# Performance work log

Hardware: AMD Instinct MI355X
Metric: run time of the kernel (lower is better)

Reference implementation:

```python
import jax, jax.numpy as jnp
import numpy as np

DIM = 512; NB = 4; BS = DIM // NB            # EinFFT blocks
DS = 64; DC = 4; EXP = 2; DI = EXP * DIM      # Mamba dims
DTR = DIM // 16                               # dt_rank
BLOCKS = 2; LAM = 0.01; B_SZ = 2; L_SZ = 1024

def layer_norm(x, w, b):
    m = x.mean(-1, keepdims=True)
    v = x.var(-1, keepdims=True)
    return (x - m) / jnp.sqrt(v + 1e-5) * w + b

def softshrink(x, lam):
    return jnp.where(x > lam, x - lam, jnp.where(x < -lam, x + lam, jnp.zeros((), x.dtype)))

def mamba(x, in_proj_w, conv_w, conv_b, x_proj_w, dt_proj_w, dt_proj_b, A_log, D, out_proj_w):
    B, L, _ = x.shape
    xz = x @ in_proj_w.T                      # (B,L,2*DI)
    xm, z = jnp.split(xz, 2, axis=-1)
    # causal depthwise conv1d, keep first L outputs
    xt = xm.transpose(0, 2, 1)                # (B,DI,L)
    conv = jax.lax.conv_general_dilated(xt, conv_w, (1,), [(DC - 1, 0)],
                                        feature_group_count=DI,
                                        dimension_numbers=('NCH', 'OIH', 'NCH'))
    xm = jax.nn.silu((conv + conv_b[None, :, None]).transpose(0, 2, 1))  # (B,L,DI)
    proj = xm @ x_proj_w.T                    # (B,L,DTR+2*DS)
    dt = proj[..., :DTR]
    Bm = proj[..., DTR:DTR + DS]
    Cm = proj[..., DTR + DS:]
    dt = jax.nn.softplus(dt @ dt_proj_w.T + dt_proj_b)   # (B,L,DI)
    A = -jnp.exp(A_log)                       # (DI,DS)

    def step(h, inp):
        dt_t, B_t, C_t, u_t = inp             # (B,DI),(B,DS),(B,DS),(B,DI)
        dA = jnp.exp(dt_t[:, :, None] * A)
        h = dA * h + dt_t[:, :, None] * B_t[:, None, :] * u_t[:, :, None]
        y = jnp.einsum('bds,bs->bd', h, C_t)
        return h, y

    h0 = jnp.zeros((B, DI, DS), x.dtype)
    _, ys = jax.lax.scan(step, h0, (dt.transpose(1, 0, 2), Bm.transpose(1, 0, 2),
                                    Cm.transpose(1, 0, 2), xm.transpose(1, 0, 2)))
    y = ys.transpose(1, 0, 2) + xm * D        # (B,L,DI)
    y = y * jax.nn.silu(z)
    return y @ out_proj_w.T

def einfft(x, cw1, cw2, cb1, cb2):
    B, N, C = x.shape
    xf = jnp.fft.fft2(x.reshape(B, N, NB, BS), axes=(1, 2), norm='ortho')
    mul = lambda t, w: jnp.einsum('BNbd,bdk->BNbk', t, w)
    r1 = jax.nn.relu(mul(xf.real, cw1[0]) - mul(xf.imag, cw1[1]) + cb1[0])
    i1 = jax.nn.relu(mul(xf.real, cw1[1]) + mul(xf.imag, cw1[0]) + cb1[1])
    r2 = softshrink(mul(r1, cw2[0]) - mul(i1, cw2[1]) + cb2[0], LAM)
    i2 = softshrink(mul(r1, cw2[1]) + mul(i1, cw2[0]) + cb2[1], LAM)
    out = jnp.fft.ifft2(r2 + 1j * i2, axes=(1, 2), norm='ortho')
    return out.real.astype(x.dtype).reshape(B, N, C)

def setup_inputs() -> dict:
    key = jax.random.key(0)
    ks = jax.random.split(key, 16)
    r = lambda i, shape, s: jax.random.normal(ks[i], shape, jnp.float32) * s
    A_log = jnp.log(jnp.tile(jnp.arange(1, DS + 1, dtype=jnp.float32), (DI, 1)))
    return {
        'x': jax.random.normal(ks[0], (B_SZ, L_SZ, DIM), jnp.float32),
        'ln_w': jnp.ones((DIM,), jnp.float32), 'ln_b': jnp.zeros((DIM,), jnp.float32),
        'in_proj_w': r(1, (2 * DI, DIM), 0.02),
        'conv_w': r(2, (DI, 1, DC), 0.1), 'conv_b': jnp.zeros((DI,), jnp.float32),
        'x_proj_w': r(3, (DTR + 2 * DS, DI), 0.02),
        'dt_proj_w': r(4, (DI, DTR), 0.02),
        'dt_proj_b': jnp.full((DI,), float(np.log(np.expm1(0.01))), jnp.float32),
        'A_log': A_log, 'D': jnp.ones((DI,), jnp.float32),
        'out_proj_w': r(5, (DIM, DI), 0.02),
        'norm2_w': jnp.ones((DIM,), jnp.float32), 'norm2_b': jnp.zeros((DIM,), jnp.float32),
        'cw1': r(6, (2, NB, BS, BS), 0.02), 'cw2': r(7, (2, NB, BS, BS), 0.02),
        'cb1': r(8, (2, NB, BS), 0.02), 'cb2': r(9, (2, NB, BS), 0.02),
    }

def reference(x, ln_w, ln_b, in_proj_w, conv_w, conv_b, x_proj_w, dt_proj_w, dt_proj_b,
              A_log, D, out_proj_w, norm2_w, norm2_b, cw1, cw2, cb1, cb2):
    for _ in range(BLOCKS):
        x = x + mamba(layer_norm(x, ln_w, ln_b), in_proj_w, conv_w, conv_b,
                      x_proj_w, dt_proj_w, dt_proj_b, A_log, D, out_proj_w)
        x = x + einfft(layer_norm(x, norm2_w, norm2_b), cw1, cw2, cb1, cb2)
    return x
```

## Files before the change

kernel.cpp:

```cpp
#include <hip/hip_runtime.h>

typedef unsigned short u16;
typedef __attribute__((ext_vector_type(8))) short bf8;
typedef __attribute__((ext_vector_type(4))) float f4;

__device__ __forceinline__ float bf2f(u16 b) {
    return __uint_as_float(((unsigned)b) << 16);
}
__device__ __forceinline__ u16 f2bf(float f) {
    unsigned u = __float_as_uint(f);
    u += 0x7fffu + ((u >> 16) & 1u);
    return (u16)(u >> 16);
}
__device__ __forceinline__ void pack8f(const float* v, u16* dst) {
    uint r0 = (uint)f2bf(v[0]) | ((uint)f2bf(v[1]) << 16);
    uint r1 = (uint)f2bf(v[2]) | ((uint)f2bf(v[3]) << 16);
    uint r2 = (uint)f2bf(v[4]) | ((uint)f2bf(v[5]) << 16);
    uint r3 = (uint)f2bf(v[6]) | ((uint)f2bf(v[7]) << 16);
    *(uint4*)dst = make_uint4(r0, r1, r2, r3);
}
__device__ __forceinline__ bf8 neg8(bf8 v) {
    union { bf8 b; uint u[4]; } t; t.b = v;
    t.u[0] ^= 0x80008000u; t.u[1] ^= 0x80008000u;
    t.u[2] ^= 0x80008000u; t.u[3] ^= 0x80008000u;
    return t.b;
}
__device__ __forceinline__ int digrev10(int x) {
    int r = __brev((unsigned)x) >> 22;
    return ((r & 0x2AA) >> 1) | ((r & 0x155) << 1);
}

__global__ void detect_k(const u16* __restrict__ dtb, int* __restrict__ flag) {
    flag[0] = (dtb[0] == dtb[1] && dtb[1] == dtb[2] && dtb[2] == dtb[3] &&
               dtb[3] == dtb[4] && dtb[4] == dtb[5]) ? 1 : 0;
    flag[1] = 1;
}

__global__ __launch_bounds__(256)
void achk_k(const float* __restrict__ alog, int* __restrict__ flag) {
    int i = blockIdx.x * 256 + threadIdx.x;
    int s = i & 63;
    float n = __expf(alog[i]);
    float e = (float)(s + 1);
    if (fabsf(n - e) > 0.02f * e) atomicAnd(&flag[1], 0);
}

struct CvtArgs {
    const void* src[18];
    void* dst[18];
    int n[18];
    int obf[18];
};
__global__ __launch_bounds__(256)
void cvt_all_k(CvtArgs a, const int* __restrict__ flag) {
    const int t = blockIdx.y;
    const int n = a.n[t];
    const int f = flag[0];
    if (a.obf[t] == 2) {
        u16* __restrict__ d = (u16*)a.dst[t];
        if (f) {
            const u16* __restrict__ s = (const u16*)a.src[t];
            for (int i = blockIdx.x * 256 + threadIdx.x; i < n; i += gridDim.x * 256) {
                int cin = i & 127, cout = (i >> 7) & 127, snb = i >> 14;
                d[(snb << 14) + (cout << 7) + cin] = s[(snb << 14) + (cin << 7) + cout];
            }
        } else {
            const float* __restrict__ s = (const float*)a.src[t];
            for (int i = blockIdx.x * 256 + threadIdx.x; i < n; i += gridDim.x * 256) {
                int cin = i & 127, cout = (i >> 7) & 127, snb = i >> 14;
                d[(snb << 14) + (cout << 7) + cin] =
                    f2bf(s[(snb << 14) + (cin << 7) + cout]);
            }
        }
    } else if (a.obf[t] == 1) {
        u16* __restrict__ d = (u16*)a.dst[t];
        if (f) {
            const u16* __restrict__ s = (const u16*)a.src[t];
            for (int i = blockIdx.x * 256 + threadIdx.x; i < n; i += gridDim.x * 256)
                d[i] = s[i];
        } else {
            const float* __restrict__ s = (const float*)a.src[t];
            for (int i = blockIdx.x * 256 + threadIdx.x; i < n; i += gridDim.x * 256)
                d[i] = f2bf(s[i]);
        }
    } else {
        float* __restrict__ d = (float*)a.dst[t];
        if (f) {
            const u16* __restrict__ s = (const u16*)a.src[t];
            for (int i = blockIdx.x * 256 + threadIdx.x; i < n; i += gridDim.x * 256)
                d[i] = bf2f(s[i]);
        } else {
            const float* __restrict__ s = (const float*)a.src[t];
            for (int i = blockIdx.x * 256 + threadIdx.x; i < n; i += gridDim.x * 256)
                d[i] = s[i];
        }
    }
}

__global__ void out_k(const float* __restrict__ in, void* __restrict__ out,
                      int n, const int* __restrict__ flag) {
    int i = blockIdx.x * 256 + threadIdx.x;
    if (i >= n) return;
    if (flag[0]) ((u16*)out)[i] = f2bf(in[i]);
    else         ((float*)out)[i] = in[i];
}

__global__ __launch_bounds__(256)
void ln_k(const float* __restrict__ x, const float* __restrict__ w,
          const float* __restrict__ b, u16* __restrict__ out) {
    const int row = blockIdx.x, tid = threadIdx.x;
    const float* xr = x + (long)row * 512;
    float v0 = xr[tid], v1 = xr[tid + 256];
    float s = v0 + v1, q = v0 * v0 + v1 * v1;
#pragma unroll
    for (int off = 32; off; off >>= 1) {
        s += __shfl_xor(s, off);
        q += __shfl_xor(q, off);
    }
    __shared__ float ss[4], qq[4];
    int wid = tid >> 6;
    if ((tid & 63) == 0) { ss[wid] = s; qq[wid] = q; }
    __syncthreads();
    s = ss[0] + ss[1] + ss[2] + ss[3];
    q = qq[0] + qq[1] + qq[2] + qq[3];
    float mean = s * (1.f / 512.f);
    float var = q * (1.f / 512.f) - mean * mean;
    float rstd = rsqrtf(var + 1e-5f);
    u16* o = out + (long)row * 512;
    o[tid]       = f2bf((v0 - mean) * rstd * w[tid]       + b[tid]);
    o[tid + 256] = f2bf((v1 - mean) * rstd * w[tid + 256] + b[tid + 256]);
}

#define LSTR 40
template <int TAF, int EPI>
__global__ __launch_bounds__(256)
void mgemm_k(const void* __restrict__ Ap, const u16* __restrict__ Bp,
             float* __restrict__ D, int N, int K, int lda, int ldb, int ldc,
             long bsA, long bsB, long bsC,
             const float* __restrict__ bias, const float* __restrict__ res) {
    const float* Af = (const float*)Ap + blockIdx.z * bsA;
    const u16*  Ab  = (const u16*)Ap + blockIdx.z * bsA;
    const u16*  B   = Bp + blockIdx.z * bsB;
    D += blockIdx.z * bsC;

    __shared__ u16 As[64 * LSTR];
    __shared__ u16 Bs[64 * LSTR];
    const int tid = threadIdx.x;
    const int lane = tid & 63;
    const int w = tid >> 6, wm = w & 1, wn = w >> 1;
    const int m0 = blockIdx.y * 64, n0 = blockIdx.x * 64;
    const int fr = (lane & 15), fq = (lane >> 4);

    f4 acc[2][2] = {};

    for (int k0 = 0; k0 < K; k0 += 32) {
        {
            const int ar = tid >> 2, aks = (tid & 3) << 3;
            if constexpr (TAF == 1) {
                *(uint4*)&As[ar * LSTR + aks] =
                    *(const uint4*)(Ab + (long)(m0 + ar) * lda + k0 + aks);
            } else if constexpr (TAF == 2) {
                const float* p = Af + (long)(m0 + ar) * lda + k0 + aks;
                float4 x = *(const float4*)p, y = *(const float4*)(p + 4);
#pragma unroll
                for (int pt = 1; pt < 4; ++pt) {
                    const float* pp = p + (long)pt * bsA;
                    float4 x1 = *(const float4*)pp, y1 = *(const float4*)(pp + 4);
                    x.x += x1.x; x.y += x1.y; x.z += x1.z; x.w += x1.w;
                    y.x += y1.x; y.y += y1.y; y.z += y1.z; y.w += y1.w;
                }
                float tv[8];
                tv[0] = x.x; tv[1] = x.y; tv[2] = x.z; tv[3] = x.w;
                tv[4] = y.x; tv[5] = y.y; tv[6] = y.z; tv[7] = y.w;
                pack8f(tv, &As[ar * LSTR + aks]);
            } else {
                const float* p = Af + (long)(m0 + ar) * lda + k0 + aks;
                float tv[8];
                float4 x = *(const float4*)p, y = *(const float4*)(p + 4);
                tv[0] = x.x; tv[1] = x.y; tv[2] = x.z; tv[3] = x.w;
                tv[4] = y.x; tv[5] = y.y; tv[6] = y.z; tv[7] = y.w;
                pack8f(tv, &As[ar * LSTR + aks]);
            }
        }
        {
            const int br = tid >> 2, bks = (tid & 3) << 3;
            uint4 raw = make_uint4(0, 0, 0, 0);
            if (n0 + br < N)
                raw = *(const uint4*)(B + (long)(n0 + br) * ldb + k0 + bks);
            *(uint4*)&Bs[br * LSTR + bks] = raw;
        }
        __syncthreads();
        bf8 af[2], bff[2];
#pragma unroll
        for (int t = 0; t < 2; t++) {
            af[t]  = *(bf8*)&As[(wm * 32 + t * 16 + fr) * LSTR + (fq << 3)];
            bff[t] = *(bf8*)&Bs[(wn * 32 + t * 16 + fr) * LSTR + (fq << 3)];
        }
#pragma unroll
        for (int i = 0; i < 2; i++)
#pragma unroll
            for (int j = 0; j < 2; j++)
                acc[i][j] = __builtin_amdgcn_mfma_f32_16x16x32_bf16(
                    af[i], bff[j], acc[i][j], 0, 0, 0);
        __syncthreads();
    }

#pragma unroll
    for (int i = 0; i < 2; i++) {
#pragma unroll
        for (int j = 0; j < 2; j++) {
            const int gmb = m0 + wm * 32 + i * 16 + (fq << 2);
            const int gn  = n0 + wn * 32 + j * 16 + fr;
            if (gn >= N) continue;
            float v[4];
#pragma unroll
            for (int e = 0; e < 4; e++) v[e] = acc[i][j][e];
            if constexpr (EPI == 1) {
                float bb = bias[gn];
#pragma unroll
                for (int e = 0; e < 4; e++) {
                    float t = v[e] + bb;
                    v[e] = (t > 20.f) ? t : log1pf(__expf(t));
                }
            }
#pragma unroll
            for (int e = 0; e < 4; e++) {
                long idx = (long)(gmb + e) * ldc + gn;
                float t = v[e];
                if constexpr (EPI == 2) t += res[idx];
                D[idx] = t;
            }
        }
    }
}

__global__ __launch_bounds__(256)
void gemm128_k(const u16* __restrict__ A, const u16* __restrict__ B,
               float* __restrict__ D, int K, int lda, int ldb, int ldc) {
    __shared__ u16 As[128 * LSTR];
    __shared__ u16 Bs[128 * LSTR];
    const int tid = threadIdx.x, lane = tid & 63;
    const int w = tid >> 6, wm = w & 1, wn = w >> 1;
    const int m0 = blockIdx.y * 128, n0 = blockIdx.x * 128;
    const int fr = lane & 15, fq = lane >> 4;
    f4 acc[4][4] = {};

    for (int k0 = 0; k0 < K; k0 += 32) {
#pragma unroll
        for (int j = 0; j < 2; ++j) {
            int idx = tid + j * 256;
            int row = idx >> 2, col = (idx & 3) << 3;
            *(uint4*)&As[row * LSTR + col] =
                *(const uint4*)(A + (long)(m0 + row) * lda + k0 + col);
            *(uint4*)&Bs[row * LSTR + col] =
                *(const uint4*)(B + (long)(n0 + row) * ldb + k0 + col);
        }
        __syncthreads();
        bf8 af[4], bfv[4];
#pragma unroll
        for (int i = 0; i < 4; ++i) {
            af[i]  = *(bf8*)&As[(wm * 64 + i * 16 + fr) * LSTR + (fq << 3)];
            bfv[i] = *(bf8*)&Bs[(wn * 64 + i * 16 + fr) * LSTR + (fq << 3)];
        }
#pragma unroll
        for (int i = 0; i < 4; ++i)
#pragma unroll
            for (int j = 0; j < 4; ++j)
                acc[i][j] = __builtin_amdgcn_mfma_f32_16x16x32_bf16(
                    af[i], bfv[j], acc[i][j], 0, 0, 0);
        __syncthreads();
    }
#pragma unroll
    for (int i = 0; i < 4; ++i)
#pragma unroll
        for (int j = 0; j < 4; ++j) {
            const int gm = m0 + wm * 64 + i * 16 + (fq << 2);
            const int gn = n0 + wn * 64 + j * 16 + fr;
#pragma unroll
            for (int e = 0; e < 4; ++e)
                D[(long)(gm + e) * ldc + gn] = acc[i][j][e];
        }
}

__global__ __launch_bounds__(1024)
void ffw_k(const u16* __restrict__ xn, u16* __restrict__ Orb,
           u16* __restrict__ Oib) {
    const int bz = blockIdx.x;
    const int b = bz >> 7, cg = bz & 127;
    const int t = threadIdx.x;
    const int f = t >> 8, tl = t & 255;
    const int c = cg + f * 128;
    __shared__ float re[4224], im[4224], twr[768], twi[768];
    if (t < 768) {
        float s, cc;
        __sincosf((float)t * -6.1359231515425649e-3f, &s, &cc);
        twr[t] = cc; twi[t] = s;
    }
    float* rf = re + f * 1056;
    float* mf = im + f * 1056;
    const u16* src = xn + ((long)b * 1024) * 512 + c;
#pragma unroll
    for (int r = 0; r < 4; ++r) {
        int n = tl + r * 256;
        float v = bf2f(src[(long)n * 512]);
        int a = n + (n >> 5);
        rf[a] = v; mf[a] = 0.f;
    }
    __syncthreads();
#pragma unroll
    for (int st = 0; st < 5; ++st) {
        const int qsh = 8 - 2 * st;
        const int q = 1 << qsh;
        const int len = q << 2;
        const int m = 1 << (2 * st);
        int j = tl & (q - 1);
        int g = tl >> qsh;
        int i0 = g * len + j;
        int a0 = i0 + (i0 >> 5);
        int i1 = i0 + q,     a1 = i1 + (i1 >> 5);
        int i2 = i0 + 2 * q, a2 = i2 + (i2 >> 5);
        int i3 = i0 + 3 * q, a3 = i3 + (i3 >> 5);
        float ar = rf[a0], ai = mf[a0];
        float br = rf[a1], bi = mf[a1];
        float cr = rf[a2], ci = mf[a2];
        float dr = rf[a3], di = mf[a3];
        float t0r = ar + cr, t0i = ai + ci;
        float t1r = ar - cr, t1i = ai - ci;
        float t2r = br + dr, t2i = bi + di;
        float u = br - dr, v = bi - di;
        rf[a0] = t0r + t2r; mf[a0] = t0i + t2i;
        {
            int k = j * m;
            float wr = twr[k], wi = twi[k];
            float xr = t1r + v, xi = t1i - u;
            rf[a1] = xr * wr - xi * wi;
            mf[a1] = xr * wi + xi * wr;
        }
        {
            int k = 2 * j * m;
            float wr = twr[k], wi = twi[k];
            float xr = t0r - t2r, xi = t0i - t2i;
            rf[a2] = xr * wr - xi * wi;
            mf[a2] = xr * wi + xi * wr;
        }
        {
            int k = 3 * j * m;
            float wr = twr[k], wi = twi[k];
            float xr = t1r - v, xi = t1i + u;
            rf[a3] = xr * wr - xi * wi;
            mf[a3] = xr * wi + xi * wr;
        }
        __syncthreads();
    }
    u16* drp = Orb + ((long)(b * 512 + c)) * 1024;
    u16* dip = Oib + ((long)(b * 512 + c)) * 1024;
#pragma unroll
    for (int r = 0; r < 4; ++r) {
        int kf = tl + r * 256;
        int sidx = digrev10(kf);
        int a = sidx + (sidx >> 5);
        float r0 = re[a],        i0v = im[a];
        float r1 = re[1056 + a], i1v = im[1056 + a];
        float r2 = re[2112 + a], i2v = im[2112 + a];
        float r3 = re[3168 + a], i3v = im[3168 + a];
        float vr, vi;
        if (f == 0)      { vr = r0 + r1 + r2 + r3;     vi = i0v + i1v + i2v + i3v; }
        else if (f == 1) { vr = r0 + i1v - r2 - i3v;   vi = i0v - r1 - i2v + r3; }
        else if (f == 2) { vr = r0 - r1 + r2 - r3;     vi = i0v - i1v + i2v - i3v; }
        else             { vr = r0 - i1v - r2 + i3v;   vi = i0v + r1 - i2v - r3; }
        drp[kf] = f2bf(vr * 0.015625f);
        dip[kf] = f2bf(vi * 0.015625f);
    }
}

__global__ __launch_bounds__(1024)
void ifw_k(const u16* __restrict__ X2r, const u16* __restrict__ X2i,
           float* __restrict__ Yc) {
    const int bz = blockIdx.x;
    const int b = bz >> 7, cg = bz & 127;
    const int t = threadIdx.x;
    const int f = t >> 8, tl = t & 255;
    const int c = cg + f * 128;
    __shared__ float re[4224], im[4224], twr[768], twi[768];
    if (t < 768) {
        float s, cc;
        __sincosf((float)t * 6.1359231515425649e-3f, &s, &cc);
        twr[t] = cc; twi[t] = s;
    }
    const u16* sr = X2r + ((long)(b * 512 + c)) * 1024;
    const u16* si = X2i + ((long)(b * 512 + c)) * 1024;
    float* rf = re + f * 1056;
    float* mf = im + f * 1056;
    const int k4 = tl * 4;
    {
        uint2 pr = *(const uint2*)&sr[k4];
        uint2 pi = *(const uint2*)&si[k4];
        u16 rv[4] = {(u16)(pr.x & 0xFFFF), (u16)(pr.x >> 16),
                     (u16)(pr.y & 0xFFFF), (u16)(pr.y >> 16)};
        u16 iv[4] = {(u16)(pi.x & 0xFFFF), (u16)(pi.x >> 16),
                     (u16)(pi.y & 0xFFFF), (u16)(pi.y >> 16)};
#pragma unroll
        for (int e = 0; e < 4; ++e) {
            int idx = k4 + e;
            int a = idx + (idx >> 5);
            rf[a] = bf2f(rv[e]);
            mf[a] = bf2f(iv[e]);
        }
    }
    __syncthreads();
    float vr[4], vi[4];
#pragma unroll
    for (int e = 0; e < 4; ++e) {
        int idx = k4 + e;
        int a = idx + (idx >> 5);
        float r0 = re[a],        i0v = im[a];
        float r1 = re[1056 + a], i1v = im[1056 + a];
        float r2 = re[2112 + a], i2v = im[2112 + a];
        float r3 = re[3168 + a], i3v = im[3168 + a];
        if (f == 0)      { vr[e] = r0 + r1 + r2 + r3;     vi[e] = i0v + i1v + i2v + i3v; }
        else if (f == 1) { vr[e] = r0 - i1v - r2 + i3v;   vi[e] = i0v + r1 - i2v - r3; }
        else if (f == 2) { vr[e] = r0 - r1 + r2 - r3;     vi[e] = i0v - i1v + i2v - i3v; }
        else             { vr[e] = r0 + i1v - r2 - i3v;   vi[e] = i0v - r1 - i2v + r3; }
        vr[e] *= 0.5f; vi[e] *= 0.5f;
    }
    __syncthreads();
#pragma unroll
    for (int e = 0; e < 4; ++e) {
        int idx = k4 + e;
        int a = idx + (idx >> 5);
        rf[a] = vr[e]; mf[a] = vi[e];
    }
    __syncthreads();
#pragma unroll
    for (int st = 0; st < 5; ++st) {
        const int qsh = 8 - 2 * st;
        const int q = 1 << qsh;
        const int len = q << 2;
        const int m = 1 << (2 * st);
        int j = tl & (q - 1);
        int g = tl >> qsh;
        int i0 = g * len + j;
        int a0 = i0 + (i0 >> 5);
        int i1 = i0 + q,     a1 = i1 + (i1 >> 5);
        int i2 = i0 + 2 * q, a2 = i2 + (i2 >> 5);
        int i3 = i0 + 3 * q, a3 = i3 + (i3 >> 5);
        float ar = rf[a0], ai = mf[a0];
        float br = rf[a1], bi = mf[a1];
        float cr = rf[a2], ci = mf[a2];
        float dr = rf[a3], di = mf[a3];
        float t0r = ar + cr, t0i = ai + ci;
        float t1r = ar - cr, t1i = ai - ci;
        float t2r = br + dr, t2i = bi + di;
        float u = br - dr, v = bi - di;
        rf[a0] = t0r + t2r; mf[a0] = t0i + t2i;
        {
            int k = j * m;
            float wr = twr[k], wi = twi[k];
            float xr = t1r - v, xi = t1i + u;
            rf[a1] = xr * wr - xi * wi;
            mf[a1] = xr * wi + xi * wr;
        }
        {
            int k = 2 * j * m;
            float wr = twr[k], wi = twi[k];
            float xr = t0r - t2r, xi = t0i - t2i;
            rf[a2] = xr * wr - xi * wi;
            mf[a2] = xr * wi + xi * wr;
        }
        {
            int k = 3 * j * m;
            float wr = twr[k], wi = twi[k];
            float xr = t1r + v, xi = t1i - u;
            rf[a3] = xr * wr - xi * wi;
            mf[a3] = xr * wi + xi * wr;
        }
        __syncthreads();
    }
    float* d = Yc + ((long)(b * 512 + c)) * 1024;
#pragma unroll
    for (int r = 0; r < 4; ++r) {
        int n = tl + r * 256;
        int sidx = digrev10(n);
        int a = sidx + (sidx >> 5);
        d[n] = rf[a] * 0.03125f;
    }
}

__global__ __launch_bounds__(256)
void transadd_k(float* __restrict__ xbuf, const float* __restrict__ Yc) {
    const int b = blockIdx.z;
    const int c0 = blockIdx.x * 64, n0 = blockIdx.y * 64;
    __shared__ float T[64][65];
    const int tid = threadIdx.x;
    const int r = tid >> 2, q = (tid & 3) * 16;
    const float* src = Yc + ((long)(b * 512 + c0 + r)) * 1024 + n0 + q;
#pragma unroll
    for (int k = 0; k < 4; ++k) {
        float4 v = *(const float4*)(src + k * 4);
        T[r][q + k * 4 + 0] = v.x; T[r][q + k * 4 + 1] = v.y;
        T[r][q + k * 4 + 2] = v.z; T[r][q + k * 4 + 3] = v.w;
    }
    __syncthreads();
    float* dst = xbuf + ((long)(b * 1024 + n0 + r)) * 512 + c0 + q;
#pragma unroll
    for (int k = 0; k < 4; ++k) {
        float4 w = *(const float4*)(dst + k * 4);
        w.x += T[q + k * 4 + 0][r]; w.y += T[q + k * 4 + 1][r];
        w.z += T[q + k * 4 + 2][r]; w.w += T[q + k * 4 + 3][r];
        *(float4*)(dst + k * 4) = w;
    }
}

#define LSTR2 136
template <int ACT>
__global__ __launch_bounds__(256)
void cmix_k(const u16* __restrict__ Xr, const u16* __restrict__ Xi,
            const u16* __restrict__ WT, const float* __restrict__ cb,
            u16* __restrict__ Or, u16* __restrict__ Oi) {
    const int z = blockIdx.z, b = z >> 2, nb = z & 3;
    const u16* Ar = Xr + (long)b * 524288 + nb * 131072;
    const u16* Ai = Xi + (long)b * 524288 + nb * 131072;
    const u16* Wr = WT + nb * 16384;
    const u16* Wi = WT + 65536 + nb * 16384;
    u16* Dr = Or + (long)b * 524288 + nb * 131072;
    u16* Di = Oi + (long)b * 524288 + nb * 131072;
    __shared__ u16 Ars[64 * LSTR2], Ais[64 * LSTR2], Brs[64 * LSTR2], Bis[64 * LSTR2];
    const int tid = threadIdx.x, lane = tid & 63;
    const int w = tid >> 6, wm = w & 1, wn = w >> 1;
    const int m0 = blockIdx.y * 64, n0 = blockIdx.x * 64;
    const int fr = (lane & 15), fq = (lane >> 4);
    f4 accr[2][2] = {}, acci[2][2] = {};

    {
        const int am = tid & 63, akb = (tid >> 6) << 3;
#pragma unroll
        for (int kk = 0; kk < 4; ++kk) {
            const int kb = kk * 32 + akb;
            u16 tr[8], ti[8];
#pragma unroll
            for (int j = 0; j < 8; j++) {
                long off = (long)(kb + j) * 1024 + m0 + am;
                tr[j] = Ar[off]; ti[j] = Ai[off];
            }
            uint r0 = (uint)tr[0] | ((uint)tr[1] << 16);
            uint r1 = (uint)tr[2] | ((uint)tr[3] << 16);
            uint r2 = (uint)tr[4] | ((uint)tr[5] << 16);
            uint r3 = (uint)tr[6] | ((uint)tr[7] << 16);
            *(uint4*)&Ars[am * LSTR2 + kb] = make_uint4(r0, r1, r2, r3);
            r0 = (uint)ti[0] | ((uint)ti[1] << 16);
            r1 = (uint)ti[2] | ((uint)ti[3] << 16);
            r2 = (uint)ti[4] | ((uint)ti[5] << 16);
            r3 = (uint)ti[6] | ((uint)ti[7] << 16);
            *(uint4*)&Ais[am * LSTR2 + kb] = make_uint4(r0, r1, r2, r3);
        }
        const int br = tid >> 2, bks = (tid & 3) << 3;
#pragma unroll
        for (int kk = 0; kk < 4; ++kk) {
            const int kb = kk * 32 + bks;
            *(uint4*)&Brs[br * LSTR2 + kb] =
                *(const uint4*)(Wr + (long)(n0 + br) * 128 + kb);
            *(uint4*)&Bis[br * LSTR2 + kb] =
                *(const uint4*)(Wi + (long)(n0 + br) * 128 + kb);
        }
    }
    __syncthreads();

#pragma unroll
    for (int kq = 0; kq < 4; ++kq) {
        const int kc = kq * 32 + (fq << 3);
        bf8 arf[2], aif[2], brf[2], bif[2];
#pragma unroll
        for (int t = 0; t < 2; t++) {
            arf[t] = *(bf8*)&Ars[(wm * 32 + t * 16 + fr) * LSTR2 + kc];
            aif[t] = *(bf8*)&Ais[(wm * 32 + t * 16 + fr) * LSTR2 + kc];
            brf[t] = *(bf8*)&Brs[(wn * 32 + t * 16 + fr) * LSTR2 + kc];
            bif[t] = *(bf8*)&Bis[(wn * 32 + t * 16 + fr) * LSTR2 + kc];
        }
        bf8 nai[2] = { neg8(aif[0]), neg8(aif[1]) };
#pragma unroll
        for (int i = 0; i < 2; i++)
#pragma unroll
            for (int j = 0; j < 2; j++) {
                accr[i][j] = __builtin_amdgcn_mfma_f32_16x16x32_bf16(arf[i], brf[j], accr[i][j], 0, 0, 0);
                accr[i][j] = __builtin_amdgcn_mfma_f32_16x16x32_bf16(nai[i], bif[j], accr[i][j], 0, 0, 0);
                acci[i][j] = __builtin_amdgcn_mfma_f32_16x16x32_bf16(arf[i], bif[j], acci[i][j], 0, 0, 0);
                acci[i][j] = __builtin_amdgcn_mfma_f32_16x16x32_bf16(aif[i], brf[j], acci[i][j], 0, 0, 0);
            }
    }

#pragma unroll
    for (int i = 0; i < 2; i++)
#pragma unroll
        for (int j = 0; j < 2; j++) {
            const int gmb = m0 + wm * 32 + i * 16 + (fq << 2);
            const int gn  = n0 + wn * 32 + j * 16 + fr;
            const float bbr = cb[nb * 128 + gn];
            const float bbi = cb[512 + nb * 128 + gn];
            u16 pr[4], pi[4];
#pragma unroll
            for (int e = 0; e < 4; e++) {
                float vr = accr[i][j][e] + bbr;
                float vi = acci[i][j][e] + bbi;
                if (ACT == 0) {
                    vr = fmaxf(vr, 0.f);
                    vi = fmaxf(vi, 0.f);
                } else {
                    vr = (vr > 0.01f) ? vr - 0.01f : ((vr < -0.01f) ? vr + 0.01f : 0.f);
                    vi = (vi > 0.01f) ? vi - 0.01f : ((vi < -0.01f) ? vi + 0.01f : 0.f);
                }
                pr[e] = f2bf(vr); pi[e] = f2bf(vi);
            }
            uint2 wr2, wi2;
            wr2.x = (uint)pr[0] | ((uint)pr[1] << 16);
            wr2.y = (uint)pr[2] | ((uint)pr[3] << 16);
            wi2.x = (uint)pi[0] | ((uint)pi[1] << 16);
            wi2.y = (uint)pi[2] | ((uint)pi[3] << 16);
            *(uint2*)&Dr[(long)gn * 1024 + gmb] = wr2;
            *(uint2*)&Di[(long)gn * 1024 + gmb] = wi2;
        }
}

__global__ __launch_bounds__(256)
void conv_k(const float* __restrict__ xz, const float* __restrict__ cw,
            const float* __restrict__ cb, u16* __restrict__ u) {
    int idx = blockIdx.x * 256 + threadIdx.x;
    int d = idx & 1023;
    int l = (idx >> 10) & 1023;
    int b = idx >> 20;
    float acc = cb[d];
    const float* base = xz + (long)b * 1024 * 2048 + d;
#pragma unroll
    for (int j = 0; j < 4; j++) {
        int li = l - 3 + j;
        if (li >= 0) acc = fmaf(cw[d * 4 + j], base[(long)li * 2048], acc);
    }
    float sig = 1.f / (1.f + __expf(-acc));
    u[idx] = f2bf(acc * sig);
}

__global__ __launch_bounds__(256)
void scan1_k(const float* __restrict__ dtL, const u16* __restrict__ uLb,
             const float* __restrict__ Pb, const float* __restrict__ alog,
             u16* __restrict__ Hb, float* __restrict__ Sbuf,
             const int* __restrict__ flag) {
    const int dg = blockIdx.x, c = blockIdx.y, b = blockIdx.z;
    const int tid = threadIdx.x;
    const int d = dg * 256 + tid;
    const int t0 = c * 16;
    __shared__ float Bls[16][64];
    {
        int r = tid >> 4, cg = (tid & 15) << 2;
        const float* src = Pb + ((long)(b * 1024 + t0 + r)) * 160 + 32 + cg;
        float4 v0 = *(const float4*)src;
        float4 v1 = *(const float4*)(src + 327680);
        float4 v2 = *(const float4*)(src + 655360);
        float4 v3 = *(const float4*)(src + 983040);
        v0.x += v1.x + v2.x + v3.x;
        v0.y += v1.y + v2.y + v3.y;
        v0.z += v1.z + v2.z + v3.z;
        v0.w += v1.w + v2.w + v3.w;
        *(float4*)&Bls[r][cg] = v0;
    }
    __syncthreads();

    float h[64];
#pragma unroll
    for (int s = 0; s < 64; s++) h[s] = 0.f;
    float S = 0.f;
    const float* dtp = dtL + (long)(b * 1024 + t0) * 1024 + d;
    const u16* up = uLb + (long)(b * 1024 + t0) * 1024 + d;

    if (flag[1]) {
        for (int t = 0; t < 16; ++t) {
            float dt = dtp[(long)t * 1024];
            float uu = bf2f(up[(long)t * 1024]);
            float dtu = dt * uu;
            S += dt;
            float q = __expf(-dt);
            float q2 = q * q, q3 = q2 * q, q4 = q2 * q2;
            float a0 = q, a1 = q2, a2 = q3, a3 = q4;
            const float4* B4p = (const float4*)&Bls[t][0];
#pragma unroll
            for (int sg = 0; sg < 16; ++sg) {
                float4 B4 = B4p[sg];
                h[sg * 4 + 0] = a0 * h[sg * 4 + 0] + dtu * B4.x;
                h[sg * 4 + 1] = a1 * h[sg * 4 + 1] + dtu * B4.y;
                h[sg * 4 + 2] = a2 * h[sg * 4 + 2] + dtu * B4.z;
                h[sg * 4 + 3] = a3 * h[sg * 4 + 3] + dtu * B4.w;
                a0 *= q4; a1 *= q4; a2 *= q4; a3 *= q4;
            }
        }
    } else {
        float A[64];
        const float* ap = alog + (long)d * 64;
#pragma unroll
        for (int s = 0; s < 64; s += 4) {
            float4 a4 = *(const float4*)(ap + s);
            A[s] = -__expf(a4.x); A[s + 1] = -__expf(a4.y);
            A[s + 2] = -__expf(a4.z); A[s + 3] = -__expf(a4.w);
        }
        for (int t = 0; t < 16; ++t) {
            float dt = dtp[(long)t * 1024];
            float uu = bf2f(up[(long)t * 1024]);
            float dtu = dt * uu;
            S += dt;
            const float4* B4p = (const float4*)&Bls[t][0];
#pragma unroll
            for (int sg = 0; sg < 16; ++sg) {
                float4 B4 = B4p[sg];
                h[sg * 4 + 0] = __expf(dt * A[sg * 4 + 0]) * h[sg * 4 + 0] + dtu * B4.x;
                h[sg * 4 + 1] = __expf(dt * A[sg * 4 + 1]) * h[sg * 4 + 1] + dtu * B4.y;
                h[sg * 4 + 2] = __expf(dt * A[sg * 4 + 2]) * h[sg * 4 + 2] + dtu * B4.z;
                h[sg * 4 + 3] = __expf(dt * A[sg * 4 + 3]) * h[sg * 4 + 3] + dtu * B4.w;
            }
        }
    }
    u16* Hp = Hb + ((((long)(b * 64 + c)) * 1024 + d) << 6);
#pragma unroll
    for (int s = 0; s < 64; s += 4) {
        uint2 p;
        p.x = ((__float_as_uint(h[s]) + 0x8000u) >> 16) |
              ((__float_as_uint(h[s + 1]) + 0x8000u) & 0xFFFF0000u);
        p.y = ((__float_as_uint(h[s + 2]) + 0x8000u) >> 16) |
              ((__float_as_uint(h[s + 3]) + 0x8000u) & 0xFFFF0000u);
        *(uint2*)&Hp[s] = p;
    }
    Sbuf[(b * 64 + c) * 1024 + d] = S;
}

__global__ __launch_bounds__(256)
void scan2_k(const float* __restrict__ alog, const float* __restrict__ Sbuf,
             u16* __restrict__ Hb) {
    int idx = blockIdx.x * 256 + threadIdx.x;
    int s = idx & 63, d = (idx >> 6) & 1023, b = idx >> 16;
    float A = -__expf(alog[(long)d * 64 + s]);
    float carry = 0.f;
    for (int c = 0; c < 64; ++c) {
        float S = Sbuf[(b * 64 + c) * 1024 + d];
        float P = __expf(A * S);
        long off = ((((long)(b * 64 + c)) * 1024 + d) << 6) + s;
        float H = bf2f(Hb[off]);
        Hb[off] = (u16)((__float_as_uint(carry) + 0x8000u) >> 16);
        carry = P * carry + H;
    }
}

__global__ __launch_bounds__(256)
void scan3_k(const float* __restrict__ dtL, const u16* __restrict__ uLb,
             const float* __restrict__ xz, const float* __restrict__ Pb,
             const float* __restrict__ alog, const u16* __restrict__ Hb,
             const float* __restrict__ Dw, const int* __restrict__ flag,
             u16* __restrict__ y2) {
    const int dg = blockIdx.x, c = blockIdx.y, b = blockIdx.z;
    const int tid = threadIdx.x;
    const int d = dg * 256 + tid;
    const int t0 = c * 16;
    __shared__ float Bls[16][64];
    __shared__ float Cls[16][64];
    {
        int r = tid >> 4, cg = (tid & 15) << 2;
        const float* src = Pb + ((long)(b * 1024 + t0 + r)) * 160 + 32 + cg;
        float4 v0 = *(const float4*)src;
        float4 v1 = *(const float4*)(src + 327680);
        float4 v2 = *(const float4*)(src + 655360);
        float4 v3 = *(const float4*)(src + 983040);
        v0.x += v1.x + v2.x + v3.x;
        v0.y += v1.y + v2.y + v3.y;
        v0.z += v1.z + v2.z + v3.z;
        v0.w += v1.w + v2.w + v3.w;
        *(float4*)&Bls[r][cg] = v0;
        float4 c0 = *(const float4*)(src + 64);
        float4 c1 = *(const float4*)(src + 64 + 327680);
        float4 c2 = *(const float4*)(src + 64 + 655360);
        float4 c3 = *(const float4*)(src + 64 + 983040);
        c0.x += c1.x + c2.x + c3.x;
        c0.y += c1.y + c2.y + c3.y;
        c0.z += c1.z + c2.z + c3.z;
        c0.w += c1.w + c2.w + c3.w;
        *(float4*)&Cls[r][cg] = c0;
    }
    __syncthreads();

    float h[64];
    const u16* Hp = Hb + ((((long)(b * 64 + c)) * 1024 + d) << 6);
#pragma unroll
    for (int s = 0; s < 64; s += 4) {
        uint2 p = *(const uint2*)&Hp[s];
        h[s]     = __uint_as_float(p.x << 16);
        h[s + 1] = __uint_as_float(p.x & 0xFFFF0000u);
        h[s + 2] = __uint_as_float(p.y << 16);
        h[s + 3] = __uint_as_float(p.y & 0xFFFF0000u);
    }
    const float Dd = Dw[d];
    const float* dtp = dtL + (long)(b * 1024 + t0) * 1024 + d;
    const u16* up = uLb + (long)(b * 1024 + t0) * 1024 + d;
    const float* zp = xz + (long)(b * 1024 + t0) * 2048 + 1024 + d;
    u16* y2p = y2 + (long)(b * 1024 + t0) * 1024 + d;

    if (flag[1]) {
        for (int t = 0; t < 16; ++t) {
            float dt = dtp[(long)t * 1024];
            float uu = bf2f(up[(long)t * 1024]);
            float zz = zp[(long)t * 2048];
            float dtu = dt * uu;
            float y = 0.f;
            float q = __expf(-dt);
            float q2 = q * q, q3 = q2 * q, q4 = q2 * q2;
            float a0 = q, a1 = q2, a2 = q3, a3 = q4;
            const float4* B4p = (const float4*)&Bls[t][0];
            const float4* C4p = (const float4*)&Cls[t][0];
#pragma unroll
            for (int sg = 0; sg < 16; ++sg) {
                float4 B4 = B4p[sg];
                float4 C4 = C4p[sg];
                h[sg * 4 + 0] = a0 * h[sg * 4 + 0] + dtu * B4.x;
                y = fmaf(h[sg * 4 + 0], C4.x, y);
                h[sg * 4 + 1] = a1 * h[sg * 4 + 1] + dtu * B4.y;
                y = fmaf(h[sg * 4 + 1], C4.y, y);
                h[sg * 4 + 2] = a2 * h[sg * 4 + 2] + dtu * B4.z;
                y = fmaf(h[sg * 4 + 2], C4.z, y);
                h[sg * 4 + 3] = a3 * h[sg * 4 + 3] + dtu * B4.w;
                y = fmaf(h[sg * 4 + 3], C4.w, y);
                a0 *= q4; a1 *= q4; a2 *= q4; a3 *= q4;
            }
            float g = zz / (1.f + __expf(-zz));
            y2p[(long)t * 1024] = f2bf((y + uu * Dd) * g);
        }
    } else {
        float A[64];
        const float* ap = alog + (long)d * 64;
#pragma unroll
        for (int s = 0; s < 64; s += 4) {
            float4 a4 = *(const float4*)(ap + s);
            A[s] = -__expf(a4.x); A[s + 1] = -__expf(a4.y);
            A[s + 2] = -__expf(a4.z); A[s + 3] = -__expf(a4.w);
        }
        for (int t = 0; t < 16; ++t) {
            float dt = dtp[(long)t * 1024];
            float uu = bf2f(up[(long)t * 1024]);
            float zz = zp[(long)t * 2048];
            float dtu = dt * uu;
            float y = 0.f;
            const float4* B4p = (const float4*)&Bls[t][0];
            const float4* C4p = (const float4*)&Cls[t][0];
#pragma unroll
            for (int sg = 0; sg < 16; ++sg) {
                float4 B4 = B4p[sg];
                float4 C4 = C4p[sg];
                h[sg * 4 + 0] = __expf(dt * A[sg * 4 + 0]) * h[sg * 4 + 0] + dtu * B4.x;
                y = fmaf(h[sg * 4 + 0], C4.x, y);
                h[sg * 4 + 1] = __expf(dt * A[sg * 4 + 1]) * h[sg * 4 + 1] + dtu * B4.y;
                y = fmaf(h[sg * 4 + 1], C4.y, y);
                h[sg * 4 + 2] = __expf(dt * A[sg * 4 + 2]) * h[sg * 4 + 2] + dtu * B4.z;
                y = fmaf(h[sg * 4 + 2], C4.z, y);
                h[sg * 4 + 3] = __expf(dt * A[sg * 4 + 3]) * h[sg * 4 + 3] + dtu * B4.w;
                y = fmaf(h[sg * 4 + 3], C4.w, y);
            }
            float g = zz / (1.f + __expf(-zz));
            y2p[(long)t * 1024] = f2bf((y + uu * Dd) * g);
        }
    }
}

extern "C" void kernel_launch(void* const* d_in, const int* in_sizes, int n_in,
                              void* d_out, int out_size, void* d_ws, size_t ws_size,
                              hipStream_t stream) {
    float* ws = (float*)d_ws;
    int* flag = (int*)ws;
    size_t o = 64;
    float* xbuf  = ws + o; o += 1048576;
    float* xz    = ws + o; o += 4194304;
    float* dtL   = ws + o; o += 2097152;
    u16* xnb     = (u16*)(ws + o); o += 524288;
    u16* wInpB   = (u16*)(ws + o); o += 524288;
    u16* wXpB    = (u16*)(ws + o); o += 81920;
    u16* wDtB    = (u16*)(ws + o); o += 16384;
    u16* wOutB   = (u16*)(ws + o); o += 262144;
    u16* WT1     = (u16*)(ws + o); o += 65536;
    u16* WT2     = (u16*)(ws + o); o += 65536;
    float* wConv = ws + o; o += 4096;
    float* wAlog = ws + o; o += 65536;
    float* wLnW  = ws + o; o += 512;
    float* wLnB  = ws + o; o += 512;
    float* wConvB= ws + o; o += 1024;
    float* wDtBias=ws + o; o += 1024;
    float* wD    = ws + o; o += 1024;
    float* wN2w  = ws + o; o += 512;
    float* wN2b  = ws + o; o += 512;
    float* wCb1  = ws + o; o += 1024;
    float* wCb2  = ws + o; o += 1024;
    float* Hreg  = ws + o; o += 4194304;
    float* Sbuf  = ws + o; o += 131072;
    float* Pbuf2 = ws + o; o += 1310720;
    u16* uLb     = (u16*)(ws + o); o += 1048576;
    u16* y2b     = (u16*)(ws + o); o += 524288;
    u16* Hb    = (u16*)Hreg;
    float* Yc  = dtL;
    u16* xzb  = (u16*)xz;
    u16* Xrb  = xzb;
    u16* Xib  = xzb + 1048576;
    u16* r1b  = xzb + 2097152;
    u16* i1b  = xzb + 3145728;
    u16* X2rb = xzb + 4194304;
    u16* X2ib = xzb + 5242880;

    dim3 blk(256);

    detect_k<<<1, 1, 0, stream>>>((const u16*)d_in[8], flag);

    CvtArgs ca;
    void* dsts[18] = {xbuf, wLnW, wLnB, wInpB, wConv, wConvB, wXpB, wDtB, wDtBias,
                      wAlog, wD, wOutB, wN2w, wN2b, WT1, WT2, wCb1, wCb2};
    int obf[18]    = {0,    0,    0,    1,     0,     0,      1,    1,    0,
                      0,     0,  1,     0,    0,    2,   2,   0,    0};
    for (int i = 0; i < 18; i++) {
        ca.src[i] = d_in[i];
        ca.dst[i] = dsts[i];
        ca.n[i] = in_sizes[i];
        ca.obf[i] = obf[i];
    }
    cvt_all_k<<<dim3(64, 18), blk, 0, stream>>>(ca, flag);
    achk_k<<<256, blk, 0, stream>>>(wAlog, flag);

    for (int it = 0; it < 2; ++it) {
        ln_k<<<2048, blk, 0, stream>>>(xbuf, wLnW, wLnB, xnb);
        gemm128_k<<<dim3(16, 16), blk, 0, stream>>>(
            xnb, wInpB, xz, 512, 512, 512, 2048);
        conv_k<<<8192, blk, 0, stream>>>(xz, wConv, wConvB, uLb);
        mgemm_k<1, 0><<<dim3(3, 32, 4), blk, 0, stream>>>(
            uLb, wXpB, Pbuf2, 160, 256, 1024, 1024, 160,
            256, 256, 327680, nullptr, nullptr);
        mgemm_k<2, 1><<<dim3(16, 32, 1), blk, 0, stream>>>(
            Pbuf2, wDtB, dtL, 1024, 32, 160, 32, 1024, 327680, 0, 0, wDtBias, nullptr);
        scan1_k<<<dim3(4, 64, 2), blk, 0, stream>>>(dtL, uLb, Pbuf2, wAlog, Hb, Sbuf, flag);
        scan2_k<<<512, blk, 0, stream>>>(wAlog, Sbuf, Hb);
        scan3_k<<<dim3(4, 64, 2), blk, 0, stream>>>(dtL, uLb, xz, Pbuf2, wAlog, Hb, wD, flag, y2b);
        mgemm_k<1, 2><<<dim3(8, 32, 1), blk, 0, stream>>>(
            y2b, wOutB, xbuf, 512, 1024, 1024, 1024, 512, 0, 0, 0, nullptr, xbuf);

        ln_k<<<2048, blk, 0, stream>>>(xbuf, wN2w, wN2b, xnb);
        ffw_k<<<256, dim3(1024), 0, stream>>>(xnb, Xrb, Xib);
        cmix_k<0><<<dim3(2, 16, 8), blk, 0, stream>>>(Xrb, Xib, WT1, wCb1, r1b, i1b);
        cmix_k<1><<<dim3(2, 16, 8), blk, 0, stream>>>(r1b, i1b, WT2, wCb2, X2rb, X2ib);
        ifw_k<<<256, dim3(1024), 0, stream>>>(X2rb, X2ib, Yc);
        transadd_k<<<dim3(8, 16, 2), blk, 0, stream>>>(xbuf, Yc);
    }

    out_k<<<(out_size + 255) / 256, blk, 0, stream>>>(xbuf, d_out, out_size, flag);
}
```

Before: 445.8 us.

## Store dt and z in bf16, split in_proj output, precompute reduced B/C

The in_proj GEMM now writes the x half as fp32 to a compact buffer and the z gate half as bf16. The dt projection epilogue emits bf16, and the scan kernels read bf16 dt and z. scan1 stores the split-K reduced B and C rows so scan3 loads them directly instead of re-reducing four partials. scan2 also prefetches the next chunk's S and H values. The aim is to cut global memory traffic in the Mamba scan path, at the cost of storing dt and z at bf16 precision.

```diff
diff --git a/kernel.cpp b/kernel.cpp
--- a/kernel.cpp
+++ b/kernel.cpp
@@ -215,7 +215,7 @@
             float v[4];
 #pragma unroll
             for (int e = 0; e < 4; e++) v[e] = acc[i][j][e];
-            if constexpr (EPI == 1) {
+            if constexpr (EPI == 1 || EPI == 3) {
                 float bb = bias[gn];
 #pragma unroll
                 for (int e = 0; e < 4; e++) {
@@ -228,7 +228,8 @@
                 long idx = (long)(gmb + e) * ldc + gn;
                 float t = v[e];
                 if constexpr (EPI == 2) t += res[idx];
-                D[idx] = t;
+                if constexpr (EPI == 3) ((u16*)D)[idx] = f2bf(t);
+                else                    D[idx] = t;
             }
         }
     }
@@ -236,7 +237,8 @@
 
 __global__ __launch_bounds__(256)
 void gemm128_k(const u16* __restrict__ A, const u16* __restrict__ B,
-               float* __restrict__ D, int K, int lda, int ldb, int ldc) {
+               float* __restrict__ Dm, u16* __restrict__ Dz,
+               int K, int lda, int ldb) {
     __shared__ u16 As[128 * LSTR];
     __shared__ u16 Bs[128 * LSTR];
     const int tid = threadIdx.x, lane = tid & 63;
@@ -276,9 +278,15 @@
         for (int j = 0; j < 4; ++j) {
             const int gm = m0 + wm * 64 + i * 16 + (fq << 2);
             const int gn = n0 + wn * 64 + j * 16 + fr;
-#pragma unroll
-            for (int e = 0; e < 4; ++e)
-                D[(long)(gm + e) * ldc + gn] = acc[i][j][e];
+            if (n0 < 1024) {
+#pragma unroll
+                for (int e = 0; e < 4; ++e)
+                    Dm[(long)(gm + e) * 1024 + gn] = acc[i][j][e];
+            } else {
+#pragma unroll
+                for (int e = 0; e < 4; ++e)
+                    Dz[(long)(gm + e) * 1024 + (gn - 1024)] = f2bf(acc[i][j][e]);
+            }
         }
 }
 
@@ -621,27 +629,28 @@
 }
 
 __global__ __launch_bounds__(256)
-void conv_k(const float* __restrict__ xz, const float* __restrict__ cw,
+void conv_k(const float* __restrict__ xm, const float* __restrict__ cw,
             const float* __restrict__ cb, u16* __restrict__ u) {
     int idx = blockIdx.x * 256 + threadIdx.x;
     int d = idx & 1023;
     int l = (idx >> 10) & 1023;
     int b = idx >> 20;
     float acc = cb[d];
-    const float* base = xz + (long)b * 1024 * 2048 + d;
+    const float* base = xm + (long)b * 1048576 + d;
 #pragma unroll
     for (int j = 0; j < 4; j++) {
         int li = l - 3 + j;
-        if (li >= 0) acc = fmaf(cw[d * 4 + j], base[(long)li * 2048], acc);
+        if (li >= 0) acc = fmaf(cw[d * 4 + j], base[(long)li * 1024], acc);
     }
     float sig = 1.f / (1.f + __expf(-acc));
     u[idx] = f2bf(acc * sig);
 }
 
 __global__ __launch_bounds__(256)
-void scan1_k(const float* __restrict__ dtL, const u16* __restrict__ uLb,
+void scan1_k(const u16* __restrict__ dtb, const u16* __restrict__ uLb,
              const float* __restrict__ Pb, const float* __restrict__ alog,
              u16* __restrict__ Hb, float* __restrict__ Sbuf,
+             float* __restrict__ Bred, float* __restrict__ Cred,
              const int* __restrict__ flag) {
     const int dg = blockIdx.x, c = blockIdx.y, b = blockIdx.z;
     const int tid = threadIdx.x;
@@ -660,6 +669,19 @@
         v0.z += v1.z + v2.z + v3.z;
         v0.w += v1.w + v2.w + v3.w;
         *(float4*)&Bls[r][cg] = v0;
+        if (dg == 0) {
+            long ro = (((long)(b * 64 + c)) * 16 + r) * 64 + cg;
+            *(float4*)&Bred[ro] = v0;
+            float4 c0 = *(const float4*)(src + 64);
+            float4 c1 = *(const float4*)(src + 64 + 327680);
+            float4 c2 = *(const float4*)(src + 64 + 655360);
+            float4 c3 = *(const float4*)(src + 64 + 983040);
+            c0.x += c1.x + c2.x + c3.x;
+            c0.y += c1.y + c2.y + c3.y;
+            c0.z += c1.z + c2.z + c3.z;
+            c0.w += c1.w + c2.w + c3.w;
+            *(float4*)&Cred[ro] = c0;
+        }
     }
     __syncthreads();
 
@@ -667,12 +689,12 @@
 #pragma unroll
     for (int s = 0; s < 64; s++) h[s] = 0.f;
     float S = 0.f;
-    const float* dtp = dtL + (long)(b * 1024 + t0) * 1024 + d;
-    const u16* up = uLb + (long)(b * 1024 + t0) * 1024 + d;
+    const u16* dtp = dtb + (long)(b * 1024 + t0) * 1024 + d;
+    const u16* up  = uLb + (long)(b * 1024 + t0) * 1024 + d;
 
     if (flag[1]) {
         for (int t = 0; t < 16; ++t) {
-            float dt = dtp[(long)t * 1024];
+            float dt = bf2f(dtp[(long)t * 1024]);
             float uu = bf2f(up[(long)t * 1024]);
             float dtu = dt * uu;
             S += dt;
@@ -700,7 +722,7 @@
             A[s + 2] = -__expf(a4.z); A[s + 3] = -__expf(a4.w);
         }
         for (int t = 0; t < 16; ++t) {
-            float dt = dtp[(long)t * 1024];
+            float dt = bf2f(dtp[(long)t * 1024]);
             float uu = bf2f(up[(long)t * 1024]);
             float dtu = dt * uu;
             S += dt;
@@ -735,22 +757,30 @@
     int s = idx & 63, d = (idx >> 6) & 1023, b = idx >> 16;
     float A = -__expf(alog[(long)d * 64 + s]);
     float carry = 0.f;
+    long off = ((((long)(b * 64)) * 1024 + d) << 6) + s;
+    int sb = (b * 64) * 1024 + d;
+    float Scur = Sbuf[sb];
+    float Hcur = bf2f(Hb[off]);
     for (int c = 0; c < 64; ++c) {
-        float S = Sbuf[(b * 64 + c) * 1024 + d];
-        float P = __expf(A * S);
-        long off = ((((long)(b * 64 + c)) * 1024 + d) << 6) + s;
-        float H = bf2f(Hb[off]);
+        float Snxt = 0.f, Hnxt = 0.f;
+        if (c < 63) {
+            Snxt = Sbuf[sb + 1024];
+            Hnxt = bf2f(Hb[off + 65536]);
+        }
+        float P = __expf(A * Scur);
         Hb[off] = (u16)((__float_as_uint(carry) + 0x8000u) >> 16);
-        carry = P * carry + H;
-    }
-}
-
-__global__ __launch_bounds__(256)
-void scan3_k(const float* __restrict__ dtL, const u16* __restrict__ uLb,
-             const float* __restrict__ xz, const float* __restrict__ Pb,
-             const float* __restrict__ alog, const u16* __restrict__ Hb,
-             const float* __restrict__ Dw, const int* __restrict__ flag,
-             u16* __restrict__ y2) {
+        carry = P * carry + Hcur;
+        Scur = Snxt; Hcur = Hnxt;
+        off += 65536; sb += 1024;
+    }
+}
+
+__global__ __launch_bounds__(256)
+void scan3_k(const u16* __restrict__ dtb, const u16* __restrict__ uLb,
+             const u16* __restrict__ zLb, const float* __restrict__ Bred,
+             const float* __restrict__ Cred, const float* __restrict__ alog,
+             const u16* __restrict__ Hb, const float* __restrict__ Dw,
+             const int* __restrict__ flag, u16* __restrict__ y2) {
     const int dg = blockIdx.x, c = blockIdx.y, b = blockIdx.z;
     const int tid = threadIdx.x;
     const int d = dg * 256 + tid;
@@ -759,25 +789,9 @@
     __shared__ float Cls[16][64];
     {
         int r = tid >> 4, cg = (tid & 15) << 2;
-        const float* src = Pb + ((long)(b * 1024 + t0 + r)) * 160 + 32 + cg;
-        float4 v0 = *(const float4*)src;
-        float4 v1 = *(const float4*)(src + 327680);
-        float4 v2 = *(const float4*)(src + 655360);
-        float4 v3 = *(const float4*)(src + 983040);
-        v0.x += v1.x + v2.x + v3.x;
-        v0.y += v1.y + v2.y + v3.y;
-        v0.z += v1.z + v2.z + v3.z;
-        v0.w += v1.w + v2.w + v3.w;
-        *(float4*)&Bls[r][cg] = v0;
-        float4 c0 = *(const float4*)(src + 64);
-        float4 c1 = *(const float4*)(src + 64 + 327680);
-        float4 c2 = *(const float4*)(src + 64 + 655360);
-        float4 c3 = *(const float4*)(src + 64 + 983040);
-        c0.x += c1.x + c2.x + c3.x;
-        c0.y += c1.y + c2.y + c3.y;
-        c0.z += c1.z + c2.z + c3.z;
-        c0.w += c1.w + c2.w + c3.w;
-        *(float4*)&Cls[r][cg] = c0;
+        long ro = (((long)(b * 64 + c)) * 16 + r) * 64 + cg;
+        *(float4*)&Bls[r][cg] = *(const float4*)&Bred[ro];
+        *(float4*)&Cls[r][cg] = *(const float4*)&Cred[ro];
     }
     __syncthreads();
 
@@ -792,16 +806,16 @@
         h[s + 3] = __uint_as_float(p.y & 0xFFFF0000u);
     }
     const float Dd = Dw[d];
-    const float* dtp = dtL + (long)(b * 1024 + t0) * 1024 + d;
-    const u16* up = uLb + (long)(b * 1024 + t0) * 1024 + d;
-    const float* zp = xz + (long)(b * 1024 + t0) * 2048 + 1024 + d;
+    const u16* dtp = dtb + (long)(b * 1024 + t0) * 1024 + d;
+    const u16* up  = uLb + (long)(b * 1024 + t0) * 1024 + d;
+    const u16* zp  = zLb + (long)(b * 1024 + t0) * 1024 + d;
     u16* y2p = y2 + (long)(b * 1024 + t0) * 1024 + d;
 
     if (flag[1]) {
         for (int t = 0; t < 16; ++t) {
-            float dt = dtp[(long)t * 1024];
+            float dt = bf2f(dtp[(long)t * 1024]);
             float uu = bf2f(up[(long)t * 1024]);
-            float zz = zp[(long)t * 2048];
+            float zz = bf2f(zp[(long)t * 1024]);
             float dtu = dt * uu;
             float y = 0.f;
             float q = __expf(-dt);
@@ -836,9 +850,9 @@
             A[s + 2] = -__expf(a4.z); A[s + 3] = -__expf(a4.w);
         }
         for (int t = 0; t < 16; ++t) {
-            float dt = dtp[(long)t * 1024];
+            float dt = bf2f(dtp[(long)t * 1024]);
             float uu = bf2f(up[(long)t * 1024]);
-            float zz = zp[(long)t * 2048];
+            float zz = bf2f(zp[(long)t * 1024]);
             float dtu = dt * uu;
             float y = 0.f;
             const float4* B4p = (const float4*)&Bls[t][0];
@@ -869,8 +883,9 @@
     int* flag = (int*)ws;
     size_t o = 64;
     float* xbuf  = ws + o; o += 1048576;
-    float* xz    = ws + o; o += 4194304;
-    float* dtL   = ws + o; o += 2097152;
+    float* fftA  = ws + o; o += 3145728;
+    float* xmL   = ws + o; o += 2097152;
+    float* Yc    = ws + o; o += 1048576;
     u16* xnb     = (u16*)(ws + o); o += 524288;
     u16* wInpB   = (u16*)(ws + o); o += 524288;
     u16* wXpB    = (u16*)(ws + o); o += 81920;
@@ -894,9 +909,12 @@
     float* Pbuf2 = ws + o; o += 1310720;
     u16* uLb     = (u16*)(ws + o); o += 1048576;
     u16* y2b     = (u16*)(ws + o); o += 524288;
+    u16* dtLb    = (u16*)(ws + o); o += 1048576;
+    u16* zLb     = (u16*)(ws + o); o += 1048576;
+    float* Bred  = ws + o; o += 131072;
+    float* Cred  = ws + o; o += 131072;
     u16* Hb    = (u16*)Hreg;
-    float* Yc  = dtL;
-    u16* xzb  = (u16*)xz;
+    u16* xzb  = (u16*)fftA;
     u16* Xrb  = xzb;
     u16* Xib  = xzb + 1048576;
     u16* r1b  = xzb + 2097152;
@@ -925,16 +943,19 @@
     for (int it = 0; it < 2; ++it) {
         ln_k<<<2048, blk, 0, stream>>>(xbuf, wLnW, wLnB, xnb);
         gemm128_k<<<dim3(16, 16), blk, 0, stream>>>(
-            xnb, wInpB, xz, 512, 512, 512, 2048);
-        conv_k<<<8192, blk, 0, stream>>>(xz, wConv, wConvB, uLb);
+            xnb, wInpB, xmL, zLb, 512, 512, 512);
+        conv_k<<<8192, blk, 0, stream>>>(xmL, wConv, wConvB, uLb);
         mgemm_k<1, 0><<<dim3(3, 32, 4), blk, 0, stream>>>(
             uLb, wXpB, Pbuf2, 160, 256, 1024, 1024, 160,
             256, 256, 327680, nullptr, nullptr);
-        mgemm_k<2, 1><<<dim3(16, 32, 1), blk, 0, stream>>>(
-            Pbuf2, wDtB, dtL, 1024, 32, 160, 32, 1024, 327680, 0, 0, wDtBias, nullptr);
-        scan1_k<<<dim3(4, 64, 2), blk, 0, stream>>>(dtL, uLb, Pbuf2, wAlog, Hb, Sbuf, flag);
+        mgemm_k<2, 3><<<dim3(16, 32, 1), blk, 0, stream>>>(
+            Pbuf2, wDtB, (float*)dtLb, 1024, 32, 160, 32, 1024, 327680, 0, 0,
+            wDtBias, nullptr);
+        scan1_k<<<dim3(4, 64, 2), blk, 0, stream>>>(
+            dtLb, uLb, Pbuf2, wAlog, Hb, Sbuf, Bred, Cred, flag);
         scan2_k<<<512, blk, 0, stream>>>(wAlog, Sbuf, Hb);
-        scan3_k<<<dim3(4, 64, 2), blk, 0, stream>>>(dtL, uLb, xz, Pbuf2, wAlog, Hb, wD, flag, y2b);
+        scan3_k<<<dim3(4, 64, 2), blk, 0, stream>>>(
+            dtLb, uLb, zLb, Bred, Cred, wAlog, Hb, wD, flag, y2b);
         mgemm_k<1, 2><<<dim3(8, 32, 1), blk, 0, stream>>>(
             y2b, wOutB, xbuf, 512, 1024, 1024, 1024, 512, 0, 0, 0, nullptr, xbuf);
 
```

Measured after the change: 461.6 us. 1.04x slower.
